# Kernel tuning notes

Measured on AMD Instinct MI355X. Metric: run time of the kernel, lower is better.

Reference implementation:

```python
import jax, jax.numpy as jnp
import numpy as np

B, S, D, H = 2, 2048, 1024, 16
DK = D // H
MAX_REL = 2047          # clip range for relative distances
REL_DIM = 64            # rel_embedding dim, summed over


def setup_inputs() -> dict:
    key = jax.random.key(0)
    ks = jax.random.split(key, 12)
    sc = 1.0 / np.sqrt(D)
    inp = {
        "q": jax.random.normal(ks[0], (B, S, D), jnp.float32),
        "k": jax.random.normal(ks[1], (B, S, D), jnp.float32),
        "v": jax.random.normal(ks[2], (B, S, D), jnp.float32),
        "Wq": jax.random.normal(ks[3], (D, D), jnp.float32) * sc,
        "bq": jnp.zeros((D,), jnp.float32),
        "Wk": jax.random.normal(ks[4], (D, D), jnp.float32) * sc,
        "bk": jnp.zeros((D,), jnp.float32),
        "Wv": jax.random.normal(ks[5], (D, D), jnp.float32) * sc,
        "bv": jnp.zeros((D,), jnp.float32),
        "Wo": jax.random.normal(ks[6], (D, D), jnp.float32) * sc,
        "bo": jnp.zeros((D,), jnp.float32),
        "rel_table": jax.random.normal(ks[7], (2 * MAX_REL + 1, REL_DIM), jnp.float32) * 0.02,
        "mask": jnp.tril(jnp.ones((1, 1, S, S), jnp.bool_)),  # causal
    }
    return inp


def reference(q, k, v, Wq, bq, Wk, bk, Wv, bv, Wo, bo, rel_table, mask):
    def split_heads(x):
        # [B,S,D] -> [B,H,S,DK]
        return x.reshape(B, -1, H, DK).transpose(0, 2, 1, 3)

    Q = split_heads(q @ Wq + bq)
    K = split_heads(k @ Wk + bk)
    V = split_heads(v @ Wv + bv)

    scores = jnp.einsum("bhqd,bhkd->bhqk", Q, K) / jnp.sqrt(jnp.float32(DK))

    # relative position bias: table[clip(j - i)] summed over rel dim -> [S,S]
    rel_idx = jnp.clip(jnp.arange(S)[None, :] - jnp.arange(S)[:, None],
                       -MAX_REL, MAX_REL) + MAX_REL
    rel_bias = rel_table[rel_idx].sum(-1)  # [S,S]
    scores = scores + rel_bias[None, None]

    scores = jnp.where(mask, scores, jnp.float32(-1e20))
    attn = jax.nn.softmax(scores, axis=-1)

    out = jnp.einsum("bhqk,bhkd->bhqd", attn, V)
    out = out.transpose(0, 2, 1, 3).reshape(B, -1, D)
    return out @ Wo + bo
```

## Files before the change

### kernel.cpp

```cpp
#include <hip/hip_runtime.h>

#define SEQ 2048
#define DIM 1024
#define NH 16
#define HD 64
#define NB 2

typedef __bf16 bf16x8 __attribute__((ext_vector_type(8)));
typedef float f32x4 __attribute__((ext_vector_type(4)));
typedef float f32x4v __attribute__((ext_vector_type(4)));
typedef float f32x4u __attribute__((ext_vector_type(4), aligned(4)));
typedef unsigned short us8 __attribute__((ext_vector_type(8)));
typedef unsigned short us4 __attribute__((ext_vector_type(4)));

#define LOG2E 1.44269504f

__device__ __forceinline__ unsigned short bfbits(float f) {
  __bf16 h = (__bf16)f;
  return __builtin_bit_cast(unsigned short, h);
}

__device__ __forceinline__ void gload16(const unsigned short* g, unsigned short* l) {
  __builtin_amdgcn_global_load_lds(
      (const __attribute__((address_space(1))) unsigned int*)(const void*)g,
      (__attribute__((address_space(3))) unsigned int*)(void*)l, 16, 0, 0);
}

__global__ __launch_bounds__(256) void wconv4_kernel(
    const float* __restrict__ W0, const float* __restrict__ W1,
    const float* __restrict__ W2, const float* __restrict__ W3,
    unsigned short* __restrict__ Wt, const float* __restrict__ rel_table,
    float* __restrict__ relsum, const float* __restrict__ Aq,
    const float* __restrict__ Ak, const float* __restrict__ Av,
    unsigned short* __restrict__ Bq, unsigned short* __restrict__ Bk,
    unsigned short* __restrict__ Bv) {
  int z = blockIdx.z;
  int tid = threadIdx.x;
  if (z == 4) {
    int ti = blockIdx.y * 16 + blockIdx.x;
    int i = ti * 256 + tid;
    if (i < 4095) {
      const f32x4v* row = reinterpret_cast<const f32x4v*>(rel_table + (size_t)i * 64);
      float s = 0.f;
      for (int d = 0; d < 16; ++d) {
        f32x4v v = row[d];
        s += v[0] + v[1] + v[2] + v[3];
      }
      relsum[i] = s * LOG2E - 8.0f;
    }
    return;
  }
  if (z >= 5) {
    const float* src = (z == 5) ? Aq : (z == 6) ? Ak : Av;
    unsigned short* dst = (z == 5) ? Bq : (z == 6) ? Bk : Bv;
    int bid2 = blockIdx.y * 16 + blockIdx.x;
    int c0 = bid2 * 256 + tid;
    for (int j = 0; j < 8; ++j) {
      size_t e = ((size_t)(c0 + j * 65536)) * 8;
      f32x4v v0 = *reinterpret_cast<const f32x4v*>(src + e);
      f32x4v v1 = *reinterpret_cast<const f32x4v*>(src + e + 4);
      us8 o;
      o[0] = bfbits(v0[0]); o[1] = bfbits(v0[1]); o[2] = bfbits(v0[2]); o[3] = bfbits(v0[3]);
      o[4] = bfbits(v1[0]); o[5] = bfbits(v1[1]); o[6] = bfbits(v1[2]); o[7] = bfbits(v1[3]);
      *reinterpret_cast<us8*>(dst + e) = o;
    }
    return;
  }
  __shared__ unsigned short T[64][68];
  const float* W = (z == 0) ? W0 : (z == 1) ? W1 : (z == 2) ? W2 : W3;
  unsigned short* out = Wt + (size_t)z * 1024 * 1024;
  int r0 = blockIdx.y * 64;
  int c0 = blockIdx.x * 64;
  for (int it = 0; it < 4; ++it) {
    int s = tid + it * 256;
    int r = s >> 4;
    int c4 = (s & 15) * 4;
    f32x4v v = *reinterpret_cast<const f32x4v*>(W + (size_t)(r0 + r) * 1024 + c0 + c4);
    us4 o;
    o[0] = bfbits(v[0]); o[1] = bfbits(v[1]); o[2] = bfbits(v[2]); o[3] = bfbits(v[3]);
    *reinterpret_cast<us4*>(&T[r][c4]) = o;
  }
  __syncthreads();
  for (int it = 0; it < 2; ++it) {
    int s = tid + it * 256;
    int n = s >> 3;
    int k8 = (s & 7) * 8;
    us8 o;
    for (int e = 0; e < 8; ++e) o[e] = T[k8 + e][n];
    *reinterpret_cast<us8*>(out + (size_t)(c0 + n) * 1024 + r0 + k8) = o;
  }
}

#define GEMM_CORE(A_, WT_)                                                   \
  __shared__ unsigned short As[2][128 * 64];                                 \
  __shared__ unsigned short Ws[2][64 * 64];                                  \
  int tid = threadIdx.x;                                                     \
  int w = tid >> 6;                                                          \
  int lane = tid & 63;                                                       \
  int lg = lane >> 4;                                                        \
  int li = lane & 15;                                                        \
  int wr = (w >> 1) * 64;                                                    \
  int wc = (w & 1) * 32;                                                     \
  int swz = li & 7;                                                          \
  f32x4 acc[4][2] = {};                                                      \
  {                                                                          \
    for (int it = 0; it < 4; ++it) {                                         \
      int s = tid + it * 256;                                                \
      int r = s >> 3, g = (s & 7) ^ (r & 7);                                 \
      gload16(A_ + (size_t)(row0 + r) * 1024 + g * 8, &As[0][s * 8]);        \
    }                                                                        \
    for (int it = 0; it < 2; ++it) {                                         \
      int s = tid + it * 256;                                                \
      int r = s >> 3, g = (s & 7) ^ (r & 7);                                 \
      gload16(WT_ + (size_t)(col0 + r) * 1024 + g * 8, &Ws[0][s * 8]);       \
    }                                                                        \
  }                                                                          \
  __syncthreads();                                                           \
  for (int ks = 0; ks < 16; ++ks) {                                          \
    if (ks < 15) {                                                           \
      int k0 = (ks + 1) * 64;                                                \
      int B2 = (ks + 1) & 1;                                                 \
      for (int it = 0; it < 4; ++it) {                                       \
        int s = tid + it * 256;                                              \
        int r = s >> 3, g = (s & 7) ^ (r & 7);                               \
        gload16(A_ + (size_t)(row0 + r) * 1024 + k0 + g * 8, &As[B2][s * 8]);\
      }                                                                      \
      for (int it = 0; it < 2; ++it) {                                       \
        int s = tid + it * 256;                                              \
        int r = s >> 3, g = (s & 7) ^ (r & 7);                               \
        gload16(WT_ + (size_t)(col0 + r) * 1024 + k0 + g * 8, &Ws[B2][s * 8]);\
      }                                                                      \
    }                                                                        \
    int B = ks & 1;                                                          \
    for (int kk = 0; kk < 2; ++kk) {                                         \
      bf16x8 af[4], bfr[2];                                                  \
      int gidx = ((kk << 2) | lg) ^ swz;                                     \
      for (int m = 0; m < 4; ++m)                                            \
        af[m] = *reinterpret_cast<const bf16x8*>(                            \
            &As[B][(wr + m * 16 + li) * 64 + gidx * 8]);                     \
      for (int n = 0; n < 2; ++n)                                            \
        bfr[n] = *reinterpret_cast<const bf16x8*>(                           \
            &Ws[B][(wc + n * 16 + li) * 64 + gidx * 8]);                     \
      for (int m = 0; m < 4; ++m)                                            \
        for (int n = 0; n < 2; ++n)                                          \
          acc[m][n] = __builtin_amdgcn_mfma_f32_16x16x32_bf16(               \
              af[m], bfr[n], acc[m][n], 0, 0, 0);                            \
    }                                                                        \
    __syncthreads();                                                         \
  }

__global__ __launch_bounds__(256) void gemm_qkv_kernel(
    const unsigned short* __restrict__ Aq, const unsigned short* __restrict__ Ak,
    const unsigned short* __restrict__ Av, const unsigned short* __restrict__ WTb,
    const float* __restrict__ bq, const float* __restrict__ bk,
    const float* __restrict__ bv, unsigned short* __restrict__ Qb,
    unsigned short* __restrict__ Kb, unsigned short* __restrict__ Vt,
    float qscale) {
  int o = (blockIdx.x & 7) * 192 + (blockIdx.x >> 3);
  int z = o >> 9;
  int r2 = o & 511;
  int row0 = (r2 >> 4) * 128;
  int col0 = (r2 & 15) * 64;
  const unsigned short* A = (z == 0) ? Aq : (z == 1) ? Ak : Av;
  const unsigned short* WT = WTb + (size_t)z * 1024 * 1024;
  const float* bias = (z == 0) ? bq : (z == 1) ? bk : bv;
  float oscale = (z == 0) ? qscale : 1.0f;

  GEMM_CORE(A, WT)

  for (int m = 0; m < 4; ++m)
    for (int n = 0; n < 2; ++n) {
      int row = row0 + wr + m * 16 + lg * 4;
      int col = col0 + wc + n * 16 + li;
      float v4[4];
      for (int r = 0; r < 4; ++r) v4[r] = (acc[m][n][r] + bias[col]) * oscale;
      if (z == 2) {
        int bb = row >> 11, seq = row & 2047;
        int hh = col >> 6, dk = col & 63;
        us4 o4;
        o4[0] = bfbits(v4[0]); o4[1] = bfbits(v4[1]);
        o4[2] = bfbits(v4[2]); o4[3] = bfbits(v4[3]);
        *reinterpret_cast<us4*>(
            Vt + ((size_t)(bb * NH + hh) * HD + dk) * SEQ + seq) = o4;
      } else {
        unsigned short* Cp = (z == 0) ? Qb : Kb;
        for (int r = 0; r < 4; ++r)
          Cp[(size_t)(row + r) * 1024 + col] = bfbits(v4[r]);
      }
    }
}

__global__ __launch_bounds__(256) void gemm_out_kernel(
    const unsigned short* __restrict__ A, const unsigned short* __restrict__ WT,
    const float* __restrict__ bias, float* __restrict__ Cp) {
  int o = ((blockIdx.x & 7) << 6) | (blockIdx.x >> 3);
  int col0 = (o & 15) * 64;
  int row0 = (o >> 4) * 128;

  GEMM_CORE(A, WT)

  for (int m = 0; m < 4; ++m)
    for (int n = 0; n < 2; ++n)
      for (int r = 0; r < 4; ++r) {
        int row = row0 + wr + m * 16 + lg * 4 + r;
        int col = col0 + wc + n * 16 + li;
        Cp[(size_t)row * 1024 + col] = acc[m][n][r] + bias[col];
      }
}

__global__ __launch_bounds__(256) void attn_kernel(
    const unsigned short* __restrict__ Qb, const unsigned short* __restrict__ Kb,
    const unsigned short* __restrict__ Vt, const float* __restrict__ relsum,
    unsigned short* __restrict__ Ob) {
  int r0_ = blockIdx.x >> 3;
  int xcd = blockIdx.x & 7;
  int qt = 31 - (r0_ >> 2);
  int bh = xcd * 4 + (r0_ & 3);
  int h = bh & 15;
  int b = bh >> 4;

  int tid = threadIdx.x;
  int w = tid >> 6;
  int lane = tid & 63;
  int lg = lane >> 4;
  int li = lane & 15;

  __shared__ unsigned short KsF[2][64 * 64];
  __shared__ unsigned short VtF[2][64 * 64];
  __shared__ __bf16 Ps[4][16][72];

  const unsigned short* kbase = Kb + ((size_t)(b)*SEQ) * DIM + h * HD;
  const unsigned short* vbase = Vt + (size_t)(b * NH + h) * HD * SEQ;

#define STAGE(TT, B)                                                        \
  {                                                                         \
    for (int it = 0; it < 2; ++it) {                                        \
      int s = tid + it * 256;                                               \
      int r = s >> 3, g = (s & 7) ^ (r & 7);                                \
      gload16(kbase + (size_t)((TT)*64 + r) * DIM + g * 8, &KsF[B][s * 8]); \
    }                                                                       \
    for (int it = 0; it < 2; ++it) {                                        \
      int s = tid + it * 256;                                               \
      int dk = s >> 3, g = (s & 7) ^ (dk & 7);                              \
      gload16(vbase + (size_t)dk * SEQ + (TT)*64 + g * 8, &VtF[B][s * 8]);  \
    }                                                                       \
  }

  int qrow = qt * 64 + w * 16 + li;
  const unsigned short* qb = Qb + ((size_t)(b * SEQ + qrow)) * DIM + h * HD;
  bf16x8 qa0 = *reinterpret_cast<const bf16x8*>(qb + lg * 8);
  bf16x8 qa1 = *reinterpret_cast<const bf16x8*>(qb + 32 + lg * 8);

  f32x4 o_acc[4] = {};
  float l_row[4] = {0.f, 0.f, 0.f, 0.f};
  int i0 = qt * 64 + w * 16 + lg * 4;
  int swz = li & 7;

  STAGE(0, 0);
  __syncthreads();

  for (int t = 0; t <= qt; ++t) {
    int B = t & 1;
    if (t < qt) STAGE(t + 1, B ^ 1);

    f32x4 s_acc[4] = {};
    __builtin_amdgcn_s_setprio(1);
    for (int kk = 0; kk < 2; ++kk) {
      bf16x8 qa = kk ? qa1 : qa0;
      int gidx = ((kk << 2) | lg) ^ swz;
      for (int n = 0; n < 4; ++n) {
        bf16x8 kb = *reinterpret_cast<const bf16x8*>(
            &KsF[B][(n * 16 + li) * 64 + gidx * 8]);
        s_acc[n] = __builtin_amdgcn_mfma_f32_16x16x32_bf16(qa, kb, s_acc[n], 0, 0, 0);
      }
    }
    __builtin_amdgcn_s_setprio(0);

    int Cbase = (t - qt) * 64 - (w * 16 + lg * 4) + li + 2047;
    if (t == qt) {
      for (int n = 0; n < 4; ++n) {
        int Cn = Cbase + n * 16;
        f32x4u rel4 = *reinterpret_cast<const f32x4u*>(&relsum[Cn - 3]);
        for (int r = 0; r < 4; ++r) {
          float sv = s_acc[n][r] + rel4[3 - r];
          sv = (Cn - r > 2047) ? -1e30f : sv;
          float e = exp2f(sv);
          s_acc[n][r] = e;
          l_row[r] += e;
        }
      }
    } else {
      for (int n = 0; n < 4; ++n) {
        int Cn = Cbase + n * 16;
        f32x4u rel4 = *reinterpret_cast<const f32x4u*>(&relsum[Cn - 3]);
        for (int r = 0; r < 4; ++r) {
          float e = exp2f(s_acc[n][r] + rel4[3 - r]);
          s_acc[n][r] = e;
          l_row[r] += e;
        }
      }
    }

    for (int n = 0; n < 4; ++n)
      for (int r = 0; r < 4; ++r)
        Ps[w][lg * 4 + r][n * 16 + li] = (__bf16)s_acc[n][r];
    asm volatile("s_waitcnt lgkmcnt(0)" ::: "memory");
    __builtin_amdgcn_sched_barrier(0);

    __builtin_amdgcn_s_setprio(1);
    for (int kk = 0; kk < 2; ++kk) {
      bf16x8 pa = *reinterpret_cast<const bf16x8*>(&Ps[w][li][kk * 32 + lg * 8]);
      int gidx = ((kk << 2) | lg) ^ swz;
      for (int n = 0; n < 4; ++n) {
        bf16x8 vb = *reinterpret_cast<const bf16x8*>(
            &VtF[B][(n * 16 + li) * 64 + gidx * 8]);
        o_acc[n] = __builtin_amdgcn_mfma_f32_16x16x32_bf16(pa, vb, o_acc[n], 0, 0, 0);
      }
    }
    __builtin_amdgcn_s_setprio(0);

    __syncthreads();
  }

  for (int msk = 1; msk < 16; msk <<= 1)
    for (int r = 0; r < 4; ++r) l_row[r] += __shfl_xor(l_row[r], msk);
  float inv_l[4];
  for (int r = 0; r < 4; ++r) inv_l[r] = 1.f / l_row[r];
  for (int n = 0; n < 4; ++n)
    for (int r = 0; r < 4; ++r) {
      int row = i0 + r;
      int dk = n * 16 + li;
      Ob[((size_t)(b * SEQ + row)) * DIM + h * HD + dk] =
          bfbits(o_acc[n][r] * inv_l[r]);
    }
#undef STAGE
}

extern "C" void kernel_launch(void* const* d_in, const int* in_sizes, int n_in,
                              void* d_out, int out_size, void* d_ws, size_t ws_size,
                              hipStream_t stream) {
  const float* q = (const float*)d_in[0];
  const float* k = (const float*)d_in[1];
  const float* v = (const float*)d_in[2];
  const float* Wq = (const float*)d_in[3];
  const float* bq = (const float*)d_in[4];
  const float* Wk = (const float*)d_in[5];
  const float* bk = (const float*)d_in[6];
  const float* Wv = (const float*)d_in[7];
  const float* bv = (const float*)d_in[8];
  const float* Wo = (const float*)d_in[9];
  const float* bo = (const float*)d_in[10];
  const float* rel = (const float*)d_in[11];

  char* ws = (char*)d_ws;
  const size_t MATB = (size_t)NB * SEQ * DIM * sizeof(unsigned short);
  const size_t WTE = (size_t)DIM * DIM;
  unsigned short* Qb = (unsigned short*)(ws);
  unsigned short* Kb = (unsigned short*)(ws + MATB);
  unsigned short* Vt = (unsigned short*)(ws + 2 * MATB);
  unsigned short* Ob = (unsigned short*)(ws + 3 * MATB);
  float* relsum = (float*)(ws + 4 * MATB);
  unsigned short* WT = (unsigned short*)(ws + 4 * MATB + 65536);

  unsigned short* Abq = (unsigned short*)d_out;
  unsigned short* Abk = (unsigned short*)d_out + (size_t)NB * SEQ * DIM;
  unsigned short* Abv = Ob;

  wconv4_kernel<<<dim3(16, 16, 8), 256, 0, stream>>>(
      Wq, Wk, Wv, Wo, WT, rel, relsum, q, k, v, Abq, Abk, Abv);

  const float qscale = 0.125f * LOG2E;
  gemm_qkv_kernel<<<dim3(1536), 256, 0, stream>>>(Abq, Abk, Abv, WT, bq, bk, bv,
                                                  Qb, Kb, Vt, qscale);

  attn_kernel<<<dim3(1024), 256, 0, stream>>>(Qb, Kb, Vt, relsum, Ob);

  gemm_out_kernel<<<dim3(512), 256, 0, stream>>>(Ob, WT + 3 * WTE, bo, (float*)d_out);
}
```

Baseline: 121.0 us.

## Enlarge attention query tile to 128 rows, two M-subtiles per wave

The attention kernel now has each block handle 128 query rows instead of 64, with every wave computing two 16-row subtiles. Each K/V tile staged in LDS and each K/V fragment read is reused across both subtiles, which halves K/V global and LDS traffic per query row. The grid shrinks from 1024 to 512 blocks. In exchange there are fewer blocks for load balance across CUs, higher register pressure from doubled accumulators, and some extra masked work on the diagonal tiles.

```diff
diff --git a/kernel.cpp b/kernel.cpp
--- a/kernel.cpp
+++ b/kernel.cpp
@@ -214,7 +214,7 @@
     unsigned short* __restrict__ Ob) {
   int r0_ = blockIdx.x >> 3;
   int xcd = blockIdx.x & 7;
-  int qt = 31 - (r0_ >> 2);
+  int qtile = 15 - (r0_ >> 2);
   int bh = xcd * 4 + (r0_ & 3);
   int h = bh & 15;
   int b = bh >> 4;
@@ -227,7 +227,7 @@
 
   __shared__ unsigned short KsF[2][64 * 64];
   __shared__ unsigned short VtF[2][64 * 64];
-  __shared__ __bf16 Ps[4][16][72];
+  __shared__ __bf16 Ps[4][32][72];
 
   const unsigned short* kbase = Kb + ((size_t)(b)*SEQ) * DIM + h * HD;
   const unsigned short* vbase = Vt + (size_t)(b * NH + h) * HD * SEQ;
@@ -246,75 +246,90 @@
     }                                                                       \
   }
 
-  int qrow = qt * 64 + w * 16 + li;
-  const unsigned short* qb = Qb + ((size_t)(b * SEQ + qrow)) * DIM + h * HD;
-  bf16x8 qa0 = *reinterpret_cast<const bf16x8*>(qb + lg * 8);
-  bf16x8 qa1 = *reinterpret_cast<const bf16x8*>(qb + 32 + lg * 8);
-
-  f32x4 o_acc[4] = {};
-  float l_row[4] = {0.f, 0.f, 0.f, 0.f};
-  int i0 = qt * 64 + w * 16 + lg * 4;
+  bf16x8 qa[2][2];
+  for (int m = 0; m < 2; ++m) {
+    int qrow = qtile * 128 + w * 32 + m * 16 + li;
+    const unsigned short* qb = Qb + ((size_t)(b * SEQ + qrow)) * DIM + h * HD;
+    qa[m][0] = *reinterpret_cast<const bf16x8*>(qb + lg * 8);
+    qa[m][1] = *reinterpret_cast<const bf16x8*>(qb + 32 + lg * 8);
+  }
+
+  f32x4 o_acc[2][4] = {};
+  float l_row[2][4] = {};
+  int i0 = qtile * 128 + w * 32 + lg * 4;
   int swz = li & 7;
+  int nkv = 2 * qtile + 2;
 
   STAGE(0, 0);
   __syncthreads();
 
-  for (int t = 0; t <= qt; ++t) {
+  for (int t = 0; t < nkv; ++t) {
     int B = t & 1;
-    if (t < qt) STAGE(t + 1, B ^ 1);
-
-    f32x4 s_acc[4] = {};
+    if (t + 1 < nkv) STAGE(t + 1, B ^ 1);
+
+    f32x4 s_acc[2][4] = {};
     __builtin_amdgcn_s_setprio(1);
     for (int kk = 0; kk < 2; ++kk) {
-      bf16x8 qa = kk ? qa1 : qa0;
       int gidx = ((kk << 2) | lg) ^ swz;
       for (int n = 0; n < 4; ++n) {
         bf16x8 kb = *reinterpret_cast<const bf16x8*>(
             &KsF[B][(n * 16 + li) * 64 + gidx * 8]);
-        s_acc[n] = __builtin_amdgcn_mfma_f32_16x16x32_bf16(qa, kb, s_acc[n], 0, 0, 0);
+        for (int m = 0; m < 2; ++m)
+          s_acc[m][n] = __builtin_amdgcn_mfma_f32_16x16x32_bf16(
+              qa[m][kk], kb, s_acc[m][n], 0, 0, 0);
       }
     }
     __builtin_amdgcn_s_setprio(0);
 
-    int Cbase = (t - qt) * 64 - (w * 16 + lg * 4) + li + 2047;
-    if (t == qt) {
-      for (int n = 0; n < 4; ++n) {
-        int Cn = Cbase + n * 16;
-        f32x4u rel4 = *reinterpret_cast<const f32x4u*>(&relsum[Cn - 3]);
-        for (int r = 0; r < 4; ++r) {
-          float sv = s_acc[n][r] + rel4[3 - r];
-          sv = (Cn - r > 2047) ? -1e30f : sv;
-          float e = exp2f(sv);
-          s_acc[n][r] = e;
-          l_row[r] += e;
+    if (t >= 2 * qtile) {
+      for (int m = 0; m < 2; ++m) {
+        int Cb = t * 64 - (i0 + m * 16) + li + 2047;
+        for (int n = 0; n < 4; ++n) {
+          int Cn = Cb + n * 16;
+          f32x4u rel4 = *reinterpret_cast<const f32x4u*>(&relsum[Cn - 3]);
+          for (int r = 0; r < 4; ++r) {
+            float sv = s_acc[m][n][r] + rel4[3 - r];
+            sv = (Cn - r > 2047) ? -1e30f : sv;
+            float e = exp2f(sv);
+            s_acc[m][n][r] = e;
+            l_row[m][r] += e;
+          }
         }
       }
     } else {
-      for (int n = 0; n < 4; ++n) {
-        int Cn = Cbase + n * 16;
-        f32x4u rel4 = *reinterpret_cast<const f32x4u*>(&relsum[Cn - 3]);
-        for (int r = 0; r < 4; ++r) {
-          float e = exp2f(s_acc[n][r] + rel4[3 - r]);
-          s_acc[n][r] = e;
-          l_row[r] += e;
+      for (int m = 0; m < 2; ++m) {
+        int Cb = t * 64 - (i0 + m * 16) + li + 2047;
+        for (int n = 0; n < 4; ++n) {
+          int Cn = Cb + n * 16;
+          f32x4u rel4 = *reinterpret_cast<const f32x4u*>(&relsum[Cn - 3]);
+          for (int r = 0; r < 4; ++r) {
+            float e = exp2f(s_acc[m][n][r] + rel4[3 - r]);
+            s_acc[m][n][r] = e;
+            l_row[m][r] += e;
+          }
         }
       }
     }
 
-    for (int n = 0; n < 4; ++n)
-      for (int r = 0; r < 4; ++r)
-        Ps[w][lg * 4 + r][n * 16 + li] = (__bf16)s_acc[n][r];
+    for (int m = 0; m < 2; ++m)
+      for (int n = 0; n < 4; ++n)
+        for (int r = 0; r < 4; ++r)
+          Ps[w][m * 16 + lg * 4 + r][n * 16 + li] = (__bf16)s_acc[m][n][r];
     asm volatile("s_waitcnt lgkmcnt(0)" ::: "memory");
     __builtin_amdgcn_sched_barrier(0);
 
     __builtin_amdgcn_s_setprio(1);
     for (int kk = 0; kk < 2; ++kk) {
-      bf16x8 pa = *reinterpret_cast<const bf16x8*>(&Ps[w][li][kk * 32 + lg * 8]);
+      bf16x8 pa[2];
+      for (int m = 0; m < 2; ++m)
+        pa[m] = *reinterpret_cast<const bf16x8*>(&Ps[w][m * 16 + li][kk * 32 + lg * 8]);
       int gidx = ((kk << 2) | lg) ^ swz;
       for (int n = 0; n < 4; ++n) {
         bf16x8 vb = *reinterpret_cast<const bf16x8*>(
             &VtF[B][(n * 16 + li) * 64 + gidx * 8]);
-        o_acc[n] = __builtin_amdgcn_mfma_f32_16x16x32_bf16(pa, vb, o_acc[n], 0, 0, 0);
+        for (int m = 0; m < 2; ++m)
+          o_acc[m][n] = __builtin_amdgcn_mfma_f32_16x16x32_bf16(
+              pa[m], vb, o_acc[m][n], 0, 0, 0);
       }
     }
     __builtin_amdgcn_s_setprio(0);
@@ -323,16 +338,19 @@
   }
 
   for (int msk = 1; msk < 16; msk <<= 1)
-    for (int r = 0; r < 4; ++r) l_row[r] += __shfl_xor(l_row[r], msk);
-  float inv_l[4];
-  for (int r = 0; r < 4; ++r) inv_l[r] = 1.f / l_row[r];
-  for (int n = 0; n < 4; ++n)
-    for (int r = 0; r < 4; ++r) {
-      int row = i0 + r;
-      int dk = n * 16 + li;
-      Ob[((size_t)(b * SEQ + row)) * DIM + h * HD + dk] =
-          bfbits(o_acc[n][r] * inv_l[r]);
-    }
+    for (int m = 0; m < 2; ++m)
+      for (int r = 0; r < 4; ++r) l_row[m][r] += __shfl_xor(l_row[m][r], msk);
+  for (int m = 0; m < 2; ++m) {
+    float inv_l[4];
+    for (int r = 0; r < 4; ++r) inv_l[r] = 1.f / l_row[m][r];
+    for (int n = 0; n < 4; ++n)
+      for (int r = 0; r < 4; ++r) {
+        int row = i0 + m * 16 + r;
+        int dk = n * 16 + li;
+        Ob[((size_t)(b * SEQ + row)) * DIM + h * HD + dk] =
+            bfbits(o_acc[m][n][r] * inv_l[r]);
+      }
+  }
 #undef STAGE
 }
 
@@ -373,7 +391,7 @@
   gemm_qkv_kernel<<<dim3(1536), 256, 0, stream>>>(Abq, Abk, Abv, WT, bq, bk, bv,
                                                   Qb, Kb, Vt, qscale);
 
-  attn_kernel<<<dim3(1024), 256, 0, stream>>>(Qb, Kb, Vt, relsum, Ob);
+  attn_kernel<<<dim3(512), 256, 0, stream>>>(Qb, Kb, Vt, relsum, Ob);
 
   gemm_out_kernel<<<dim3(512), 256, 0, stream>>>(Ob, WT + 3 * WTE, bo, (float*)d_out);
 }
```

Measured after the change: 139.0 us. 14.9% more time.
